# Optimization experiments

Measured on AMD Instinct MI355X. Metric: run time of the kernel, lower is better.

## Reference

```python
import jax, jax.numpy as jnp
import numpy as np

E = 384      # n_embed
H = 6        # n_head
HS = E // H  # head_size = 64
B = 64
T = 256      # == block_size
FF = 4 * E


def _layernorm(x, g, b, eps=1e-5):
    m = x.mean(-1, keepdims=True)
    v = ((x - m) ** 2).mean(-1, keepdims=True)
    return (x - m) / jnp.sqrt(v + eps) * g + b


def _mha(q_in, k_in, v_in, wq, bq, wk, bk, wv, bv, pw, pb):
    # Faithful to source: scale uses q_in's last dim (n_embed=384), NOT head_size,
    # and the causal tril mask is applied even in cross-attention.
    scale = q_in.shape[-1] ** -0.5
    q = jnp.einsum('bte,hes->bhts', q_in, wq) + bq[None, :, None, :]  # [B,H,T1,HS]
    k = jnp.einsum('bue,hes->bhus', k_in, wk) + bk[None, :, None, :]  # [B,H,T2,HS]
    v = jnp.einsum('bue,hes->bhus', v_in, wv) + bv[None, :, None, :]
    wei = jnp.einsum('bhts,bhus->bhtu', q, k) * scale                 # [B,H,T1,T2]
    T1, T2 = q_in.shape[1], k_in.shape[1]
    mask = jnp.tril(jnp.ones((T1, T2), dtype=bool))
    wei = jnp.where(mask[None, None], wei, -jnp.inf)
    wei = jax.nn.softmax(wei, axis=-1)
    out = jnp.einsum('bhtu,bhus->bths', wei, v)                       # [B,T1,H,HS]
    out = out.reshape(out.shape[0], out.shape[1], -1)                 # concat heads
    return out @ pw + pb


def setup_inputs() -> dict:
    key = jax.random.key(0)
    ks = jax.random.split(key, 32)
    s = 0.02
    d = {
        'encode_output': jax.random.normal(ks[0], (B, T, E), jnp.float32),
        'x': jax.random.normal(ks[1], (B, T, E), jnp.float32),
    }
    i = 2
    for p in ('sa1', 'sa2'):
        d[p + '_wq'] = jax.random.normal(ks[i], (H, E, HS), jnp.float32) * s; i += 1
        d[p + '_bq'] = jnp.zeros((H, HS), jnp.float32)
        d[p + '_wk'] = jax.random.normal(ks[i], (H, E, HS), jnp.float32) * s; i += 1
        d[p + '_bk'] = jnp.zeros((H, HS), jnp.float32)
        d[p + '_wv'] = jax.random.normal(ks[i], (H, E, HS), jnp.float32) * s; i += 1
        d[p + '_bv'] = jnp.zeros((H, HS), jnp.float32)
        d[p + '_pw'] = jax.random.normal(ks[i], (E, E), jnp.float32) * s; i += 1
        d[p + '_pb'] = jnp.zeros((E,), jnp.float32)
    d['ff_w1'] = jax.random.normal(ks[i], (E, FF), jnp.float32) * s; i += 1
    d['ff_b1'] = jnp.zeros((FF,), jnp.float32)
    d['ff_w2'] = jax.random.normal(ks[i], (FF, E), jnp.float32) * s; i += 1
    d['ff_b2'] = jnp.zeros((E,), jnp.float32)
    for n in ('ln1', 'ln2', 'ln3'):
        d[n + '_g'] = jnp.ones((E,), jnp.float32)
        d[n + '_b'] = jnp.zeros((E,), jnp.float32)
    return d


def reference(encode_output, x,
              sa1_wq, sa1_bq, sa1_wk, sa1_bk, sa1_wv, sa1_bv, sa1_pw, sa1_pb,
              sa2_wq, sa2_bq, sa2_wk, sa2_bk, sa2_wv, sa2_bv, sa2_pw, sa2_pb,
              ff_w1, ff_b1, ff_w2, ff_b2,
              ln1_g, ln1_b, ln2_g, ln2_b, ln3_g, ln3_b):
    # masked self-attention + add&norm
    a1 = _mha(x, x, x, sa1_wq, sa1_bq, sa1_wk, sa1_bk, sa1_wv, sa1_bv, sa1_pw, sa1_pb)
    o1 = _layernorm(x + a1, ln1_g, ln1_b)
    # cross-attention (q=o1, k=v=encode_output) + add&norm
    a2 = _mha(o1, encode_output, encode_output,
              sa2_wq, sa2_bq, sa2_wk, sa2_bk, sa2_wv, sa2_bv, sa2_pw, sa2_pb)
    o2 = _layernorm(o1 + a2, ln2_g, ln2_b)
    # FFN + add&norm
    f = jax.nn.relu(o2 @ ff_w1 + ff_b1) @ ff_w2 + ff_b2
    return _layernorm(o2 + f, ln3_g, ln3_b)
```

## Files before the change

kernel.cpp:

```cpp
#include <hip/hip_runtime.h>

typedef __attribute__((ext_vector_type(8))) short bf16x8;
typedef __attribute__((ext_vector_type(4))) float f32x4;

__device__ __forceinline__ float b2f(ushort b) {
    union { unsigned int u; float f; } x;
    x.u = ((unsigned int)b) << 16;
    return x.f;
}
__device__ __forceinline__ ushort f2b(float f) {
    union { float f; unsigned int u; } x;
    x.f = f;
    unsigned int r = x.u + 0x7fffu + ((x.u >> 16) & 1u);
    return (ushort)(r >> 16);
}
__device__ __forceinline__ int4 pack8(float4 a, float4 b) {
    union { int4 v; ushort u[8]; } r;
    r.u[0] = f2b(a.x); r.u[1] = f2b(a.y); r.u[2] = f2b(a.z); r.u[3] = f2b(a.w);
    r.u[4] = f2b(b.x); r.u[5] = f2b(b.y); r.u[6] = f2b(b.z); r.u[7] = f2b(b.w);
    return r.v;
}
__device__ __forceinline__ int4 add_resb(int4 cs, int4 rs) {
    const ushort* c = (const ushort*)&cs; const ushort* r = (const ushort*)&rs;
    union { int4 v; ushort u[8]; } o;
#pragma unroll
    for (int j = 0; j < 8; j++) o.u[j] = f2b(b2f(c[j]) + b2f(r[j]));
    return o.v;
}
__device__ __forceinline__ int4 add_resf(int4 cs, float4 r0, float4 r1) {
    const ushort* c = (const ushort*)&cs;
    const float* rf0 = (const float*)&r0; const float* rf1 = (const float*)&r1;
    union { int4 v; ushort u[8]; } o;
#pragma unroll
    for (int j = 0; j < 4; j++) o.u[j] = f2b(b2f(c[j]) + rf0[j]);
#pragma unroll
    for (int j = 0; j < 4; j++) o.u[4 + j] = f2b(b2f(c[4 + j]) + rf1[j]);
    return o.v;
}

__global__ __launch_bounds__(256) void gemm_bt(
    const ushort* __restrict__ A, const ushort* __restrict__ Bt,
    ushort* __restrict__ C, const float* __restrict__ bias,
    const ushort* __restrict__ resb, const float* __restrict__ resf,
    int N, int K, int relu)
{
    __shared__ __align__(16) ushort As[128 * 32];
    __shared__ __align__(16) ushort Bs[128 * 32];
    __shared__ __align__(16) ushort Cs[64 * 132];
    const int tid  = threadIdx.x;
    const int wave = tid >> 6, lane = tid & 63;
    const int wm = wave >> 1, wn = wave & 1;
    const int qd = lane >> 4, lc = lane & 15;
    const int id = blockIdx.x, xcd = id & 7, sub = id >> 3;
    const int row0 = (xcd * 16 + (sub & 15)) * 128;
    const int col0 = (sub >> 4) * 128;

    const int srow = tid >> 1;
    const int scol = (tid & 1) * 16;
    const ushort* Ag = A  + (size_t)(row0 + srow) * K + scol;
    const ushort* Bg = Bt + (size_t)(col0 + srow) * K + scol;
    ushort* Asd = &As[srow * 32 + scol];
    ushort* Bsd = &Bs[srow * 32 + scol];

    f32x4 acc[4][4];
#pragma unroll
    for (int i = 0; i < 4; i++)
#pragma unroll
        for (int j = 0; j < 4; j++) acc[i][j] = 0.0f;

    int4 a0 = *(const int4*)(Ag);
    int4 a1 = *(const int4*)(Ag + 8);
    int4 b0 = *(const int4*)(Bg);
    int4 b1 = *(const int4*)(Bg + 8);

    for (int k0 = 0; k0 < K; k0 += 32) {
        __syncthreads();
        *(int4*)Asd = a0; *(int4*)(Asd + 8) = a1;
        *(int4*)Bsd = b0; *(int4*)(Bsd + 8) = b1;
        if (k0 + 32 < K) {
            a0 = *(const int4*)(Ag + k0 + 32);
            a1 = *(const int4*)(Ag + k0 + 40);
            b0 = *(const int4*)(Bg + k0 + 32);
            b1 = *(const int4*)(Bg + k0 + 40);
        }
        __syncthreads();

        bf16x8 af[4], bfr[4];
#pragma unroll
        for (int mi = 0; mi < 4; mi++)
            af[mi] = *(const bf16x8*)&As[(wm * 64 + mi * 16 + lc) * 32 + qd * 8];
#pragma unroll
        for (int ni = 0; ni < 4; ni++)
            bfr[ni] = *(const bf16x8*)&Bs[(wn * 64 + ni * 16 + lc) * 32 + qd * 8];
#pragma unroll
        for (int mi = 0; mi < 4; mi++)
#pragma unroll
            for (int ni = 0; ni < 4; ni++)
                acc[mi][ni] = __builtin_amdgcn_mfma_f32_16x16x32_bf16(
                    af[mi], bfr[ni], acc[mi][ni], 0, 0, 0);
    }

#pragma unroll
    for (int half = 0; half < 2; half++) {
        __syncthreads();
        if (wm == half) {
#pragma unroll
            for (int mi = 0; mi < 4; mi++)
#pragma unroll
                for (int r = 0; r < 4; r++) {
                    int lr = mi * 16 + qd * 4 + r;
#pragma unroll
                    for (int ni = 0; ni < 4; ni++) {
                        float v = acc[mi][ni][r];
                        if (bias) v += bias[col0 + wn * 64 + ni * 16 + lc];
                        if (relu) v = fmaxf(v, 0.0f);
                        Cs[lr * 132 + wn * 64 + ni * 16 + lc] = f2b(v);
                    }
                }
        }
        __syncthreads();
        int lr = tid >> 2, cc = (tid & 3) * 32;
        size_t base = (size_t)(row0 + half * 64 + lr) * N + col0 + cc;
#pragma unroll
        for (int i = 0; i < 4; i++) {
            int4 d = *(const int4*)&Cs[lr * 132 + cc + i * 8];
            if (resb) d = add_resb(d, *(const int4*)&resb[base + i * 8]);
            else if (resf) d = add_resf(d, *(const float4*)&resf[base + i * 8],
                                           *(const float4*)&resf[base + i * 8 + 4]);
            *(int4*)&C[base + i * 8] = d;
        }
    }
}

__global__ __launch_bounds__(256) void gemm_n64(
    const ushort* __restrict__ A, const ushort* __restrict__ Bt,
    ushort* __restrict__ C, const float* __restrict__ bias,
    const ushort* __restrict__ resb, const float* __restrict__ resf,
    int N, int K, int relu)
{
    __shared__ __align__(16) ushort As[128 * 32];
    __shared__ __align__(16) ushort Bs[64 * 32];
    __shared__ __align__(16) ushort Cs[128 * 68];
    const int tid  = threadIdx.x;
    const int wave = tid >> 6, lane = tid & 63;
    const int qd = lane >> 4, lc = lane & 15;
    const int id = blockIdx.x, xcd = id & 7, sub = id >> 3;
    const int row0 = (xcd * 16 + (sub & 15)) * 128;
    const int col0 = (sub >> 4) * 64;

    const int srow = tid >> 1;
    const int scol = (tid & 1) * 16;
    const ushort* Ag = A + (size_t)(row0 + srow) * K + scol;
    ushort* Asd = &As[srow * 32 + scol];
    const int brow = tid >> 2;
    const int bcol = (tid & 3) * 8;
    const ushort* Bg = Bt + (size_t)(col0 + brow) * K + bcol;
    ushort* Bsd = &Bs[brow * 32 + bcol];

    f32x4 acc[2][4];
#pragma unroll
    for (int i = 0; i < 2; i++)
#pragma unroll
        for (int j = 0; j < 4; j++) acc[i][j] = 0.0f;

    int4 a0 = *(const int4*)(Ag);
    int4 a1 = *(const int4*)(Ag + 8);
    int4 b0 = *(const int4*)(Bg);

    for (int k0 = 0; k0 < K; k0 += 32) {
        __syncthreads();
        *(int4*)Asd = a0; *(int4*)(Asd + 8) = a1;
        *(int4*)Bsd = b0;
        if (k0 + 32 < K) {
            a0 = *(const int4*)(Ag + k0 + 32);
            a1 = *(const int4*)(Ag + k0 + 40);
            b0 = *(const int4*)(Bg + k0 + 32);
        }
        __syncthreads();

        bf16x8 af[2], bfr[4];
#pragma unroll
        for (int mi = 0; mi < 2; mi++)
            af[mi] = *(const bf16x8*)&As[(wave * 32 + mi * 16 + lc) * 32 + qd * 8];
#pragma unroll
        for (int ni = 0; ni < 4; ni++)
            bfr[ni] = *(const bf16x8*)&Bs[(ni * 16 + lc) * 32 + qd * 8];
#pragma unroll
        for (int mi = 0; mi < 2; mi++)
#pragma unroll
            for (int ni = 0; ni < 4; ni++)
                acc[mi][ni] = __builtin_amdgcn_mfma_f32_16x16x32_bf16(
                    af[mi], bfr[ni], acc[mi][ni], 0, 0, 0);
    }

    __syncthreads();
#pragma unroll
    for (int mi = 0; mi < 2; mi++)
#pragma unroll
        for (int r = 0; r < 4; r++) {
            int lr = wave * 32 + mi * 16 + qd * 4 + r;
#pragma unroll
            for (int ni = 0; ni < 4; ni++) {
                float v = acc[mi][ni][r];
                if (bias) v += bias[col0 + ni * 16 + lc];
                if (relu) v = fmaxf(v, 0.0f);
                Cs[lr * 68 + ni * 16 + lc] = f2b(v);
            }
        }
    __syncthreads();
    {
        int lr = tid >> 1, cc = (tid & 1) * 32;
        size_t base = (size_t)(row0 + lr) * N + col0 + cc;
#pragma unroll
        for (int i = 0; i < 4; i++) {
            int4 d = *(const int4*)&Cs[lr * 68 + cc + i * 8];
            if (resb) d = add_resb(d, *(const int4*)&resb[base + i * 8]);
            else if (resf) d = add_resf(d, *(const float4*)&resf[base + i * 8],
                                           *(const float4*)&resf[base + i * 8 + 4]);
            *(int4*)&C[base + i * 8] = d;
        }
    }
}

__global__ __launch_bounds__(256) void gemm_dual(
    const ushort* __restrict__ A1, const ushort* __restrict__ B1t,
    ushort* __restrict__ C1, const float* __restrict__ bias1, int N1,
    const ushort* __restrict__ A2, const ushort* __restrict__ B2t,
    ushort* __restrict__ C2, const float* __restrict__ bias2, int N2,
    int split, int K)
{
    __shared__ __align__(16) ushort As[128 * 32];
    __shared__ __align__(16) ushort Bs[64 * 32];
    __shared__ __align__(16) ushort Cs[128 * 68];
    const int tid  = threadIdx.x;
    const int wave = tid >> 6, lane = tid & 63;
    const int qd = lane >> 4, lc = lane & 15;
    const int id = blockIdx.x, xcd = id & 7, sub = id >> 3;
    const int row0 = (xcd * 16 + (sub & 15)) * 128;
    int ct = sub >> 4;
    const bool first = ct < split;
    const ushort* A  = first ? A1 : A2;
    const ushort* Bt = first ? B1t : B2t;
    ushort* C        = first ? C1 : C2;
    const float* bias = first ? bias1 : bias2;
    const int N      = first ? N1 : N2;
    const int col0   = (first ? ct : ct - split) * 64;

    const int srow = tid >> 1;
    const int scol = (tid & 1) * 16;
    const ushort* Ag = A + (size_t)(row0 + srow) * K + scol;
    ushort* Asd = &As[srow * 32 + scol];
    const int brow = tid >> 2;
    const int bcol = (tid & 3) * 8;
    const ushort* Bg = Bt + (size_t)(col0 + brow) * K + bcol;
    ushort* Bsd = &Bs[brow * 32 + bcol];

    f32x4 acc[2][4];
#pragma unroll
    for (int i = 0; i < 2; i++)
#pragma unroll
        for (int j = 0; j < 4; j++) acc[i][j] = 0.0f;

    int4 a0 = *(const int4*)(Ag);
    int4 a1 = *(const int4*)(Ag + 8);
    int4 b0 = *(const int4*)(Bg);

    for (int k0 = 0; k0 < K; k0 += 32) {
        __syncthreads();
        *(int4*)Asd = a0; *(int4*)(Asd + 8) = a1;
        *(int4*)Bsd = b0;
        if (k0 + 32 < K) {
            a0 = *(const int4*)(Ag + k0 + 32);
            a1 = *(const int4*)(Ag + k0 + 40);
            b0 = *(const int4*)(Bg + k0 + 32);
        }
        __syncthreads();

        bf16x8 af[2], bfr[4];
#pragma unroll
        for (int mi = 0; mi < 2; mi++)
            af[mi] = *(const bf16x8*)&As[(wave * 32 + mi * 16 + lc) * 32 + qd * 8];
#pragma unroll
        for (int ni = 0; ni < 4; ni++)
            bfr[ni] = *(const bf16x8*)&Bs[(ni * 16 + lc) * 32 + qd * 8];
#pragma unroll
        for (int mi = 0; mi < 2; mi++)
#pragma unroll
            for (int ni = 0; ni < 4; ni++)
                acc[mi][ni] = __builtin_amdgcn_mfma_f32_16x16x32_bf16(
                    af[mi], bfr[ni], acc[mi][ni], 0, 0, 0);
    }

    __syncthreads();
#pragma unroll
    for (int mi = 0; mi < 2; mi++)
#pragma unroll
        for (int r = 0; r < 4; r++) {
            int lr = wave * 32 + mi * 16 + qd * 4 + r;
#pragma unroll
            for (int ni = 0; ni < 4; ni++)
                Cs[lr * 68 + ni * 16 + lc] = f2b(acc[mi][ni][r] + bias[col0 + ni * 16 + lc]);
        }
    __syncthreads();
    {
        int lr = tid >> 1, cc = (tid & 1) * 32;
        size_t base = (size_t)(row0 + lr) * N + col0 + cc;
#pragma unroll
        for (int i = 0; i < 4; i++)
            *(int4*)&C[base + i * 8] = *(const int4*)&Cs[lr * 68 + cc + i * 8];
    }
}

__global__ __launch_bounds__(256) void attn(
    const ushort* __restrict__ q, int qstr,
    const ushort* __restrict__ k, int kstr,
    const ushort* __restrict__ v, int vstr,
    ushort* __restrict__ out)
{
    __shared__ __align__(16) ushort Qs[64 * 72];
    __shared__ __align__(16) ushort Kc[64 * 72];
    __shared__ __align__(16) ushort Vc[64 * 72];
    __shared__ __align__(16) ushort Ps[64 * 264];

    const int tid = threadIdx.x;
    const int wave = tid >> 6, lane = tid & 63;
    const int qd = lane >> 4, lc = lane & 15;
    const int b = blockIdx.z, h = blockIdx.y, t0 = blockIdx.x * 64;
    const int hc = h * 64;
    const float scale = 0.051031036307982884f;

    {
        int r = tid >> 2, c = (tid & 3) * 16;
        int4 q0 = *(const int4*)&q[(size_t)(b * 256 + t0 + r) * qstr + hc + c];
        int4 q1 = *(const int4*)&q[(size_t)(b * 256 + t0 + r) * qstr + hc + c + 8];
        *(int4*)&Qs[r * 72 + c] = q0;
        *(int4*)&Qs[r * 72 + c + 8] = q1;
    }

    f32x4 accS[16];
#pragma unroll
    for (int j = 0; j < 16; j++) accS[j] = 0.0f;

    for (int uc = 0; uc < 4; uc++) {
        int r = tid >> 2, c = (tid & 3) * 16;
        int4 k0v = *(const int4*)&k[(size_t)(b * 256 + uc * 64 + r) * kstr + hc + c];
        int4 k1v = *(const int4*)&k[(size_t)(b * 256 + uc * 64 + r) * kstr + hc + c + 8];
        __syncthreads();
        *(int4*)&Kc[r * 72 + c] = k0v;
        *(int4*)&Kc[r * 72 + c + 8] = k1v;
        __syncthreads();
#pragma unroll
        for (int s0 = 0; s0 < 64; s0 += 32) {
            bf16x8 a = *(const bf16x8*)&Qs[(wave * 16 + lc) * 72 + s0 + qd * 8];
#pragma unroll
            for (int ni = 0; ni < 4; ni++) {
                bf16x8 bb = *(const bf16x8*)&Kc[(ni * 16 + lc) * 72 + s0 + qd * 8];
                accS[uc * 4 + ni] =
                    __builtin_amdgcn_mfma_f32_16x16x32_bf16(a, bb, accS[uc * 4 + ni], 0, 0, 0);
            }
        }
    }

#pragma unroll
    for (int rr = 0; rr < 4; rr++) {
        int t = t0 + wave * 16 + qd * 4 + rr;
        float pv[16];
        float mx = -3.0e38f;
#pragma unroll
        for (int j = 0; j < 16; j++) {
            int u = (j >> 2) * 64 + (j & 3) * 16 + lc;
            float s = accS[j][rr] * scale;
            s = (u <= t) ? s : -3.0e38f;
            pv[j] = s;
            mx = fmaxf(mx, s);
        }
#pragma unroll
        for (int m = 1; m < 16; m <<= 1) mx = fmaxf(mx, __shfl_xor(mx, m, 16));
        float sum = 0.0f;
#pragma unroll
        for (int j = 0; j < 16; j++) { float p = __expf(pv[j] - mx); pv[j] = p; sum += p; }
#pragma unroll
        for (int m = 1; m < 16; m <<= 1) sum += __shfl_xor(sum, m, 16);
        float inv = 1.0f / sum;
#pragma unroll
        for (int j = 0; j < 16; j++) {
            int u = (j >> 2) * 64 + (j & 3) * 16 + lc;
            Ps[(wave * 16 + qd * 4 + rr) * 264 + u] = f2b(pv[j] * inv);
        }
    }

    f32x4 accO[4];
#pragma unroll
    for (int j = 0; j < 4; j++) accO[j] = 0.0f;
    for (int uc = 0; uc < 4; uc++) {
        int r = tid >> 2, s0 = (tid & 3) * 16;
        int4 v0 = *(const int4*)&v[(size_t)(b * 256 + uc * 64 + r) * vstr + hc + s0];
        int4 v1 = *(const int4*)&v[(size_t)(b * 256 + uc * 64 + r) * vstr + hc + s0 + 8];
        __syncthreads();
        {
            const ushort* t0p = (const ushort*)&v0;
            const ushort* t1p = (const ushort*)&v1;
#pragma unroll
            for (int j = 0; j < 8; j++) Vc[(s0 + j) * 72 + r] = t0p[j];
#pragma unroll
            for (int j = 0; j < 8; j++) Vc[(s0 + 8 + j) * 72 + r] = t1p[j];
        }
        __syncthreads();
#pragma unroll
        for (int u0 = 0; u0 < 64; u0 += 32) {
            bf16x8 a = *(const bf16x8*)&Ps[(wave * 16 + lc) * 264 + uc * 64 + u0 + qd * 8];
#pragma unroll
            for (int ni = 0; ni < 4; ni++) {
                bf16x8 bb = *(const bf16x8*)&Vc[(ni * 16 + lc) * 72 + u0 + qd * 8];
                accO[ni] = __builtin_amdgcn_mfma_f32_16x16x32_bf16(a, bb, accO[ni], 0, 0, 0);
            }
        }
    }

#pragma unroll
    for (int ni = 0; ni < 4; ni++)
#pragma unroll
        for (int rr = 0; rr < 4; rr++) {
            int t = t0 + wave * 16 + qd * 4 + rr;
            out[(size_t)(b * 256 + t) * 384 + hc + ni * 16 + lc] = f2b(accO[ni][rr]);
        }
}

__global__ __launch_bounds__(256) void lnorm(
    const ushort* __restrict__ in, const float* __restrict__ g,
    const float* __restrict__ be, ushort* __restrict__ outb,
    float* __restrict__ outf)
{
    const int wave = threadIdx.x >> 6, lane = threadIdx.x & 63;
    const int row = blockIdx.x * 4 + wave;
    const ushort* r = in + (size_t)row * 384;
    float x[6], s1 = 0.0f, s2 = 0.0f;
#pragma unroll
    for (int j = 0; j < 6; j++) {
        x[j] = b2f(r[j * 64 + lane]);
        s1 += x[j]; s2 += x[j] * x[j];
    }
#pragma unroll
    for (int m = 1; m < 64; m <<= 1) {
        s1 += __shfl_xor(s1, m, 64);
        s2 += __shfl_xor(s2, m, 64);
    }
    float mean = s1 * (1.0f / 384.0f);
    float var  = s2 * (1.0f / 384.0f) - mean * mean;
    float rstd = rsqrtf(var + 1e-5f);
#pragma unroll
    for (int j = 0; j < 6; j++) {
        float y = (x[j] - mean) * rstd * g[j * 64 + lane] + be[j * 64 + lane];
        if (outb) outb[(size_t)row * 384 + j * 64 + lane] = f2b(y);
        if (outf) outf[(size_t)row * 384 + j * 64 + lane] = y;
    }
}

__device__ __forceinline__ void dev_cvt(const float* in, ushort* out, int blk) {
    size_t i = ((size_t)blk * 256 + threadIdx.x) * 8;
    float4 a = *(const float4*)(in + i);
    float4 b = *(const float4*)(in + i + 4);
    *(int4*)(out + i) = pack8(a, b);
}
__device__ __forceinline__ void dev_transp(const float* in, ushort* out,
                                           int R, int C, int bx, int by,
                                           float (*t)[33]) {
    const int tx = threadIdx.x & 31, ty = threadIdx.x >> 5;
    const int c0 = bx * 32, r0 = by * 32;
#pragma unroll
    for (int i = 0; i < 32; i += 8)
        t[ty + i][tx] = in[(size_t)(r0 + ty + i) * C + c0 + tx];
    __syncthreads();
#pragma unroll
    for (int i = 0; i < 32; i += 8)
        out[(size_t)(c0 + ty + i) * R + r0 + tx] = f2b(t[tx][ty + i]);
}
__device__ __forceinline__ void dev_packqkv(const float* wq, const float* wk,
                                            const float* wv, ushort* Wt,
                                            int blk, float (*t)[33]) {
    const int tx = threadIdx.x & 31, ty = threadIdx.x >> 5;
    const int bx = blk % 12, by = (blk / 12) % 2, bz = blk / 24;
    const int e0 = bx * 32, s0 = by * 32;
    const int seg = bz / 6, h = bz - seg * 6;
    const float* w = (seg == 0) ? wq : (seg == 1) ? wk : wv;
    const float* wh = w + (size_t)h * 384 * 64;
#pragma unroll
    for (int i = 0; i < 32; i += 8)
        t[ty + i][tx] = wh[(size_t)(e0 + ty + i) * 64 + s0 + tx];
    __syncthreads();
    const int nbase = seg * 384 + h * 64 + s0;
#pragma unroll
    for (int i = 0; i < 32; i += 8)
        Wt[(size_t)(nbase + ty + i) * 384 + e0 + tx] = f2b(t[tx][ty + i]);
}

__global__ __launch_bounds__(256) void prep_all(
    const float* __restrict__ x, ushort* __restrict__ xb,
    const float* __restrict__ enc, ushort* __restrict__ encb,
    const float* __restrict__ s1wq, const float* __restrict__ s1wk,
    const float* __restrict__ s1wv, ushort* __restrict__ W1,
    const float* __restrict__ s2wq, const float* __restrict__ s2wk,
    const float* __restrict__ s2wv, ushort* __restrict__ W2,
    const float* __restrict__ s1pw, ushort* __restrict__ pw1t,
    const float* __restrict__ s2pw, ushort* __restrict__ pw2t,
    const float* __restrict__ fw1, ushort* __restrict__ w1t,
    const float* __restrict__ fw2, ushort* __restrict__ w2t,
    const float* __restrict__ s1bq, const float* __restrict__ s1bk,
    const float* __restrict__ s1bv, const float* __restrict__ s2bq,
    const float* __restrict__ s2bk, const float* __restrict__ s2bv,
    float* __restrict__ bias1, float* __restrict__ bias2)
{
    __shared__ float t[32][33];
    int blk = blockIdx.x;
    if (blk < 3072) { dev_cvt(x, xb, blk); return; }
    blk -= 3072;
    if (blk < 3072) { dev_cvt(enc, encb, blk); return; }
    blk -= 3072;
    if (blk < 432) { dev_packqkv(s1wq, s1wk, s1wv, W1, blk, t); return; }
    blk -= 432;
    if (blk < 432) { dev_packqkv(s2wq, s2wk, s2wv, W2, blk, t); return; }
    blk -= 432;
    if (blk < 144) { dev_transp(s1pw, pw1t, 384, 384, blk % 12, blk / 12, t); return; }
    blk -= 144;
    if (blk < 144) { dev_transp(s2pw, pw2t, 384, 384, blk % 12, blk / 12, t); return; }
    blk -= 144;
    if (blk < 576) { dev_transp(fw1, w1t, 384, 1536, blk % 48, blk / 48, t); return; }
    blk -= 576;
    if (blk < 576) { dev_transp(fw2, w2t, 1536, 384, blk % 12, blk / 12, t); return; }
    blk -= 576;
    int i = blk * 256 + threadIdx.x;
    if (i >= 2304) return;
    int grp = i / 1152, r = i - grp * 1152;
    int seg = r / 384, nn = r - seg * 384;
    const float* src = grp == 0 ? (seg == 0 ? s1bq : seg == 1 ? s1bk : s1bv)
                                : (seg == 0 ? s2bq : seg == 1 ? s2bk : s2bv);
    (grp == 0 ? bias1 : bias2)[r] = src[nn];
}

extern "C" void kernel_launch(void* const* d_in, const int* in_sizes, int n_in,
                              void* d_out, int out_size, void* d_ws, size_t ws_size,
                              hipStream_t stream)
{
    const float* enc = (const float*)d_in[0];
    const float* x   = (const float*)d_in[1];
    const float* s1wq = (const float*)d_in[2];  const float* s1bq = (const float*)d_in[3];
    const float* s1wk = (const float*)d_in[4];  const float* s1bk = (const float*)d_in[5];
    const float* s1wv = (const float*)d_in[6];  const float* s1bv = (const float*)d_in[7];
    const float* s1pw = (const float*)d_in[8];  const float* s1pb = (const float*)d_in[9];
    const float* s2wq = (const float*)d_in[10]; const float* s2bq = (const float*)d_in[11];
    const float* s2wk = (const float*)d_in[12]; const float* s2bk = (const float*)d_in[13];
    const float* s2wv = (const float*)d_in[14]; const float* s2bv = (const float*)d_in[15];
    const float* s2pw = (const float*)d_in[16]; const float* s2pb = (const float*)d_in[17];
    const float* fw1 = (const float*)d_in[18];  const float* fb1 = (const float*)d_in[19];
    const float* fw2 = (const float*)d_in[20];  const float* fb2 = (const float*)d_in[21];
    const float* g1 = (const float*)d_in[22];   const float* be1 = (const float*)d_in[23];
    const float* g2 = (const float*)d_in[24];   const float* be2 = (const float*)d_in[25];
    const float* g3 = (const float*)d_in[26];   const float* be3 = (const float*)d_in[27];

    if (ws_size < 80216064u) return;

    ushort* wsp = (ushort*)d_ws;
    ushort* qkv1 = wsp;
    ushort* q2   = wsp;
    ushort* kv2  = wsp + 6291456;
    ushort* h1   = wsp;
    ushort* att  = wsp + 18874368;
    ushort* xb   = wsp + 18874368;
    ushort* tmp  = wsp + 25165824;
    ushort* o1b  = wsp + 31457280;
    ushort* W1   = wsp + 37748736;
    ushort* W2   = W1 + 442368;
    ushort* pw1t = W2 + 442368;
    ushort* pw2t = pw1t + 147456;
    ushort* w1t  = pw2t + 147456;
    ushort* w2t  = w1t + 589824;

    ushort* encb = (ushort*)d_out;
    ushort* o2b  = (ushort*)d_out;
    float* bias1 = (float*)((ushort*)d_out + 6291456);
    float* bias2 = bias1 + 1152;

    prep_all<<<dim3(8457), dim3(256), 0, stream>>>(
        x, xb, enc, encb,
        s1wq, s1wk, s1wv, W1, s2wq, s2wk, s2wv, W2,
        s1pw, pw1t, s2pw, pw2t, fw1, w1t, fw2, w2t,
        s1bq, s1bk, s1bv, s2bq, s2bk, s2bv, bias1, bias2);

    gemm_bt<<<dim3(9 * 128), dim3(256), 0, stream>>>(xb, W1, qkv1, bias1, nullptr, nullptr, 1152, 384, 0);
    attn<<<dim3(4, 6, 64), dim3(256), 0, stream>>>(qkv1, 1152, qkv1 + 384, 1152, qkv1 + 768, 1152, att);
    gemm_n64<<<dim3(6 * 128), dim3(256), 0, stream>>>(att, pw1t, tmp, s1pb, nullptr, x, 384, 384, 0);
    lnorm<<<dim3(4096), dim3(256), 0, stream>>>(tmp, g1, be1, o1b, nullptr);

    gemm_dual<<<dim3(18 * 128), dim3(256), 0, stream>>>(
        o1b, W2, q2, bias2, 384,
        encb, W2 + 147456, kv2, bias2 + 384, 768, 6, 384);
    attn<<<dim3(4, 6, 64), dim3(256), 0, stream>>>(q2, 384, kv2, 768, kv2 + 384, 768, att);
    gemm_n64<<<dim3(6 * 128), dim3(256), 0, stream>>>(att, pw2t, tmp, s2pb, o1b, nullptr, 384, 384, 0);
    lnorm<<<dim3(4096), dim3(256), 0, stream>>>(tmp, g2, be2, o2b, nullptr);

    gemm_bt<<<dim3(12 * 128), dim3(256), 0, stream>>>(o2b, w1t, h1, fb1, nullptr, nullptr, 1536, 384, 1);
    gemm_n64<<<dim3(6 * 128), dim3(256), 0, stream>>>(h1, w2t, tmp, fb2, o2b, nullptr, 384, 1536, 0);
    lnorm<<<dim3(4096), dim3(256), 0, stream>>>(tmp, g3, be3, nullptr, (float*)d_out);
}
```

Baseline: 455.7 us.

## Use direct global-to-LDS loads with double-buffered K tiles in GEMMs

The three GEMM kernels stop staging A/B tiles through registers and instead issue global_load_lds so data goes straight into shared memory. Each kernel gets two LDS buffers and prefetches the next K tile while the current one feeds the MFMAs, using explicit vmcnt waits and raw barriers. The epilogue's output staging buffer is aliased onto the same LDS region. This removes the register round trip and the VGPR pressure of the prefetch, but leans on hand-counted vmcnt and barrier ordering for correctness.

```diff
diff --git a/kernel.cpp b/kernel.cpp
--- a/kernel.cpp
+++ b/kernel.cpp
@@ -36,6 +36,12 @@
 #pragma unroll
     for (int j = 0; j < 4; j++) o.u[4 + j] = f2b(b2f(c[4 + j]) + rf1[j]);
     return o.v;
+}
+
+__device__ __forceinline__ void gll16(const ushort* g, ushort* l) {
+    __builtin_amdgcn_global_load_lds(
+        (__attribute__((address_space(1))) void*)(g),
+        (__attribute__((address_space(3))) void*)(l), 16, 0, 0);
 }
 
 __global__ __launch_bounds__(256) void gemm_bt(
@@ -44,9 +50,7 @@
     const ushort* __restrict__ resb, const float* __restrict__ resf,
     int N, int K, int relu)
 {
-    __shared__ __align__(16) ushort As[128 * 32];
-    __shared__ __align__(16) ushort Bs[128 * 32];
-    __shared__ __align__(16) ushort Cs[64 * 132];
+    __shared__ __align__(16) ushort sm[16384];
     const int tid  = threadIdx.x;
     const int wave = tid >> 6, lane = tid & 63;
     const int wm = wave >> 1, wn = wave & 1;
@@ -55,12 +59,13 @@
     const int row0 = (xcd * 16 + (sub & 15)) * 128;
     const int col0 = (sub >> 4) * 128;
 
-    const int srow = tid >> 1;
-    const int scol = (tid & 1) * 16;
-    const ushort* Ag = A  + (size_t)(row0 + srow) * K + scol;
-    const ushort* Bg = Bt + (size_t)(col0 + srow) * K + scol;
-    ushort* Asd = &As[srow * 32 + scol];
-    ushort* Bsd = &Bs[srow * 32 + scol];
+    const int crow = lane >> 2, ccol = (lane & 3) * 8;
+    const ushort* Ag0 = A  + (size_t)(row0 + wave * 32 + crow) * K + ccol;
+    const ushort* Ag1 = Ag0 + (size_t)16 * K;
+    const ushort* Bg0 = Bt + (size_t)(col0 + wave * 32 + crow) * K + ccol;
+    const ushort* Bg1 = Bg0 + (size_t)16 * K;
+    ushort* dA = &sm[wave * 1024];
+    ushort* dB = &sm[4096 + wave * 1024];
 
     f32x4 acc[4][4];
 #pragma unroll
@@ -68,38 +73,43 @@
 #pragma unroll
         for (int j = 0; j < 4; j++) acc[i][j] = 0.0f;
 
-    int4 a0 = *(const int4*)(Ag);
-    int4 a1 = *(const int4*)(Ag + 8);
-    int4 b0 = *(const int4*)(Bg);
-    int4 b1 = *(const int4*)(Bg + 8);
-
-    for (int k0 = 0; k0 < K; k0 += 32) {
-        __syncthreads();
-        *(int4*)Asd = a0; *(int4*)(Asd + 8) = a1;
-        *(int4*)Bsd = b0; *(int4*)(Bsd + 8) = b1;
-        if (k0 + 32 < K) {
-            a0 = *(const int4*)(Ag + k0 + 32);
-            a1 = *(const int4*)(Ag + k0 + 40);
-            b0 = *(const int4*)(Bg + k0 + 32);
-            b1 = *(const int4*)(Bg + k0 + 40);
-        }
-        __syncthreads();
-
+    gll16(Ag0, dA); gll16(Ag1, dA + 512);
+    gll16(Bg0, dB); gll16(Bg1, dB + 512);
+
+    const int NT = K >> 5;
+    int cur = 0;
+    for (int t = 0; t < NT; ++t) {
+        __builtin_amdgcn_s_barrier();
+        if (t + 1 < NT) {
+            const int ko = (t + 1) << 5;
+            const int bo = (cur ^ 1) * 8192;
+            gll16(Ag0 + ko, dA + bo); gll16(Ag1 + ko, dA + bo + 512);
+            gll16(Bg0 + ko, dB + bo); gll16(Bg1 + ko, dB + bo + 512);
+            asm volatile("s_waitcnt vmcnt(4)" ::: "memory");
+        } else {
+            asm volatile("s_waitcnt vmcnt(0)" ::: "memory");
+        }
+        __builtin_amdgcn_s_barrier();
+
+        const ushort* Ac = &sm[cur * 8192];
+        const ushort* Bc = &sm[cur * 8192 + 4096];
         bf16x8 af[4], bfr[4];
 #pragma unroll
         for (int mi = 0; mi < 4; mi++)
-            af[mi] = *(const bf16x8*)&As[(wm * 64 + mi * 16 + lc) * 32 + qd * 8];
+            af[mi] = *(const bf16x8*)&Ac[(wm * 64 + mi * 16 + lc) * 32 + qd * 8];
 #pragma unroll
         for (int ni = 0; ni < 4; ni++)
-            bfr[ni] = *(const bf16x8*)&Bs[(wn * 64 + ni * 16 + lc) * 32 + qd * 8];
+            bfr[ni] = *(const bf16x8*)&Bc[(wn * 64 + ni * 16 + lc) * 32 + qd * 8];
 #pragma unroll
         for (int mi = 0; mi < 4; mi++)
 #pragma unroll
             for (int ni = 0; ni < 4; ni++)
                 acc[mi][ni] = __builtin_amdgcn_mfma_f32_16x16x32_bf16(
                     af[mi], bfr[ni], acc[mi][ni], 0, 0, 0);
-    }
-
+        cur ^= 1;
+    }
+
+    ushort* Cs = sm;
 #pragma unroll
     for (int half = 0; half < 2; half++) {
         __syncthreads();
@@ -138,9 +148,7 @@
     const ushort* __restrict__ resb, const float* __restrict__ resf,
     int N, int K, int relu)
 {
-    __shared__ __align__(16) ushort As[128 * 32];
-    __shared__ __align__(16) ushort Bs[64 * 32];
-    __shared__ __align__(16) ushort Cs[128 * 68];
+    __shared__ __align__(16) ushort sm[12288];
     const int tid  = threadIdx.x;
     const int wave = tid >> 6, lane = tid & 63;
     const int qd = lane >> 4, lc = lane & 15;
@@ -148,14 +156,12 @@
     const int row0 = (xcd * 16 + (sub & 15)) * 128;
     const int col0 = (sub >> 4) * 64;
 
-    const int srow = tid >> 1;
-    const int scol = (tid & 1) * 16;
-    const ushort* Ag = A + (size_t)(row0 + srow) * K + scol;
-    ushort* Asd = &As[srow * 32 + scol];
-    const int brow = tid >> 2;
-    const int bcol = (tid & 3) * 8;
-    const ushort* Bg = Bt + (size_t)(col0 + brow) * K + bcol;
-    ushort* Bsd = &Bs[brow * 32 + bcol];
+    const int crow = lane >> 2, ccol = (lane & 3) * 8;
+    const ushort* Ag0 = A  + (size_t)(row0 + wave * 32 + crow) * K + ccol;
+    const ushort* Ag1 = Ag0 + (size_t)16 * K;
+    const ushort* Bg0 = Bt + (size_t)(col0 + wave * 16 + crow) * K + ccol;
+    ushort* dA = &sm[wave * 1024];
+    ushort* dB = &sm[4096 + wave * 512];
 
     f32x4 acc[2][4];
 #pragma unroll
@@ -163,36 +169,43 @@
 #pragma unroll
         for (int j = 0; j < 4; j++) acc[i][j] = 0.0f;
 
-    int4 a0 = *(const int4*)(Ag);
-    int4 a1 = *(const int4*)(Ag + 8);
-    int4 b0 = *(const int4*)(Bg);
-
-    for (int k0 = 0; k0 < K; k0 += 32) {
-        __syncthreads();
-        *(int4*)Asd = a0; *(int4*)(Asd + 8) = a1;
-        *(int4*)Bsd = b0;
-        if (k0 + 32 < K) {
-            a0 = *(const int4*)(Ag + k0 + 32);
-            a1 = *(const int4*)(Ag + k0 + 40);
-            b0 = *(const int4*)(Bg + k0 + 32);
-        }
-        __syncthreads();
-
+    gll16(Ag0, dA); gll16(Ag1, dA + 512);
+    gll16(Bg0, dB);
+
+    const int NT = K >> 5;
+    int cur = 0;
+    for (int t = 0; t < NT; ++t) {
+        __builtin_amdgcn_s_barrier();
+        if (t + 1 < NT) {
+            const int ko = (t + 1) << 5;
+            const int bo = (cur ^ 1) * 6144;
+            gll16(Ag0 + ko, dA + bo); gll16(Ag1 + ko, dA + bo + 512);
+            gll16(Bg0 + ko, dB + bo);
+            asm volatile("s_waitcnt vmcnt(3)" ::: "memory");
+        } else {
+            asm volatile("s_waitcnt vmcnt(0)" ::: "memory");
+        }
+        __builtin_amdgcn_s_barrier();
+
+        const ushort* Ac = &sm[cur * 6144];
+        const ushort* Bc = &sm[cur * 6144 + 4096];
         bf16x8 af[2], bfr[4];
 #pragma unroll
         for (int mi = 0; mi < 2; mi++)
-            af[mi] = *(const bf16x8*)&As[(wave * 32 + mi * 16 + lc) * 32 + qd * 8];
+            af[mi] = *(const bf16x8*)&Ac[(wave * 32 + mi * 16 + lc) * 32 + qd * 8];
 #pragma unroll
         for (int ni = 0; ni < 4; ni++)
-            bfr[ni] = *(const bf16x8*)&Bs[(ni * 16 + lc) * 32 + qd * 8];
+            bfr[ni] = *(const bf16x8*)&Bc[(ni * 16 + lc) * 32 + qd * 8];
 #pragma unroll
         for (int mi = 0; mi < 2; mi++)
 #pragma unroll
             for (int ni = 0; ni < 4; ni++)
                 acc[mi][ni] = __builtin_amdgcn_mfma_f32_16x16x32_bf16(
                     af[mi], bfr[ni], acc[mi][ni], 0, 0, 0);
-    }
-
+        cur ^= 1;
+    }
+
+    ushort* Cs = sm;
     __syncthreads();
 #pragma unroll
     for (int mi = 0; mi < 2; mi++)
@@ -229,9 +242,7 @@
     ushort* __restrict__ C2, const float* __restrict__ bias2, int N2,
     int split, int K)
 {
-    __shared__ __align__(16) ushort As[128 * 32];
-    __shared__ __align__(16) ushort Bs[64 * 32];
-    __shared__ __align__(16) ushort Cs[128 * 68];
+    __shared__ __align__(16) ushort sm[12288];
     const int tid  = threadIdx.x;
     const int wave = tid >> 6, lane = tid & 63;
     const int qd = lane >> 4, lc = lane & 15;
@@ -246,14 +257,12 @@
     const int N      = first ? N1 : N2;
     const int col0   = (first ? ct : ct - split) * 64;
 
-    const int srow = tid >> 1;
-    const int scol = (tid & 1) * 16;
-    const ushort* Ag = A + (size_t)(row0 + srow) * K + scol;
-    ushort* Asd = &As[srow * 32 + scol];
-    const int brow = tid >> 2;
-    const int bcol = (tid & 3) * 8;
-    const ushort* Bg = Bt + (size_t)(col0 + brow) * K + bcol;
-    ushort* Bsd = &Bs[brow * 32 + bcol];
+    const int crow = lane >> 2, ccol = (lane & 3) * 8;
+    const ushort* Ag0 = A  + (size_t)(row0 + wave * 32 + crow) * K + ccol;
+    const ushort* Ag1 = Ag0 + (size_t)16 * K;
+    const ushort* Bg0 = Bt + (size_t)(col0 + wave * 16 + crow) * K + ccol;
+    ushort* dA = &sm[wave * 1024];
+    ushort* dB = &sm[4096 + wave * 512];
 
     f32x4 acc[2][4];
 #pragma unroll
@@ -261,36 +270,43 @@
 #pragma unroll
         for (int j = 0; j < 4; j++) acc[i][j] = 0.0f;
 
-    int4 a0 = *(const int4*)(Ag);
-    int4 a1 = *(const int4*)(Ag + 8);
-    int4 b0 = *(const int4*)(Bg);
-
-    for (int k0 = 0; k0 < K; k0 += 32) {
-        __syncthreads();
-        *(int4*)Asd = a0; *(int4*)(Asd + 8) = a1;
-        *(int4*)Bsd = b0;
-        if (k0 + 32 < K) {
-            a0 = *(const int4*)(Ag + k0 + 32);
-            a1 = *(const int4*)(Ag + k0 + 40);
-            b0 = *(const int4*)(Bg + k0 + 32);
-        }
-        __syncthreads();
-
+    gll16(Ag0, dA); gll16(Ag1, dA + 512);
+    gll16(Bg0, dB);
+
+    const int NT = K >> 5;
+    int cur = 0;
+    for (int t = 0; t < NT; ++t) {
+        __builtin_amdgcn_s_barrier();
+        if (t + 1 < NT) {
+            const int ko = (t + 1) << 5;
+            const int bo = (cur ^ 1) * 6144;
+            gll16(Ag0 + ko, dA + bo); gll16(Ag1 + ko, dA + bo + 512);
+            gll16(Bg0 + ko, dB + bo);
+            asm volatile("s_waitcnt vmcnt(3)" ::: "memory");
+        } else {
+            asm volatile("s_waitcnt vmcnt(0)" ::: "memory");
+        }
+        __builtin_amdgcn_s_barrier();
+
+        const ushort* Ac = &sm[cur * 6144];
+        const ushort* Bc = &sm[cur * 6144 + 4096];
         bf16x8 af[2], bfr[4];
 #pragma unroll
         for (int mi = 0; mi < 2; mi++)
-            af[mi] = *(const bf16x8*)&As[(wave * 32 + mi * 16 + lc) * 32 + qd * 8];
+            af[mi] = *(const bf16x8*)&Ac[(wave * 32 + mi * 16 + lc) * 32 + qd * 8];
 #pragma unroll
         for (int ni = 0; ni < 4; ni++)
-            bfr[ni] = *(const bf16x8*)&Bs[(ni * 16 + lc) * 32 + qd * 8];
+            bfr[ni] = *(const bf16x8*)&Bc[(ni * 16 + lc) * 32 + qd * 8];
 #pragma unroll
         for (int mi = 0; mi < 2; mi++)
 #pragma unroll
             for (int ni = 0; ni < 4; ni++)
                 acc[mi][ni] = __builtin_amdgcn_mfma_f32_16x16x32_bf16(
                     af[mi], bfr[ni], acc[mi][ni], 0, 0, 0);
-    }
-
+        cur ^= 1;
+    }
+
+    ushort* Cs = sm;
     __syncthreads();
 #pragma unroll
     for (int mi = 0; mi < 2; mi++)
```

Result: no change. 452.0 us (-0.8%).

## Rewrite GEMMs to stage full-K weight slab in LDS via direct global loads

Applied to the files above, without the earlier changes.

Replaces the per-32-K double-buffered A/B LDS tiling with a scheme that loads a 64-column weight slab covering 384 K into LDS through global_load_lds. A fragments are read straight from global memory into registers. Each wave now writes its own epilogue tile, so the block-wide barrier before the store goes away, and MFMA sections get raised scheduling priority. This cuts per-K-step barriers and LDS traffic for A, at the cost of uncoalesced, possibly latency-exposed A loads from global memory and larger LDS use per block.

```diff
diff --git a/kernel.cpp b/kernel.cpp
--- a/kernel.cpp
+++ b/kernel.cpp
@@ -38,206 +38,114 @@
     return o.v;
 }
 
-__global__ __launch_bounds__(256) void gemm_bt(
+__device__ __forceinline__ void gll16(const ushort* g, ushort* l) {
+    __builtin_amdgcn_global_load_lds(
+        (__attribute__((address_space(1))) void*)(g),
+        (__attribute__((address_space(3))) void*)(l), 16, 0, 0);
+}
+
+template<int MI>
+__global__ __launch_bounds__(256) void gemm_bs(
     const ushort* __restrict__ A, const ushort* __restrict__ Bt,
     ushort* __restrict__ C, const float* __restrict__ bias,
     const ushort* __restrict__ resb, const float* __restrict__ resf,
     int N, int K, int relu)
 {
-    __shared__ __align__(16) ushort As[128 * 32];
-    __shared__ __align__(16) ushort Bs[128 * 32];
-    __shared__ __align__(16) ushort Cs[64 * 132];
-    const int tid  = threadIdx.x;
-    const int wave = tid >> 6, lane = tid & 63;
-    const int wm = wave >> 1, wn = wave & 1;
-    const int qd = lane >> 4, lc = lane & 15;
-    const int id = blockIdx.x, xcd = id & 7, sub = id >> 3;
-    const int row0 = (xcd * 16 + (sub & 15)) * 128;
-    const int col0 = (sub >> 4) * 128;
-
-    const int srow = tid >> 1;
-    const int scol = (tid & 1) * 16;
-    const ushort* Ag = A  + (size_t)(row0 + srow) * K + scol;
-    const ushort* Bg = Bt + (size_t)(col0 + srow) * K + scol;
-    ushort* Asd = &As[srow * 32 + scol];
-    ushort* Bsd = &Bs[srow * 32 + scol];
-
-    f32x4 acc[4][4];
-#pragma unroll
-    for (int i = 0; i < 4; i++)
-#pragma unroll
-        for (int j = 0; j < 4; j++) acc[i][j] = 0.0f;
-
-    int4 a0 = *(const int4*)(Ag);
-    int4 a1 = *(const int4*)(Ag + 8);
-    int4 b0 = *(const int4*)(Bg);
-    int4 b1 = *(const int4*)(Bg + 8);
-
-    for (int k0 = 0; k0 < K; k0 += 32) {
-        __syncthreads();
-        *(int4*)Asd = a0; *(int4*)(Asd + 8) = a1;
-        *(int4*)Bsd = b0; *(int4*)(Bsd + 8) = b1;
-        if (k0 + 32 < K) {
-            a0 = *(const int4*)(Ag + k0 + 32);
-            a1 = *(const int4*)(Ag + k0 + 40);
-            b0 = *(const int4*)(Bg + k0 + 32);
-            b1 = *(const int4*)(Bg + k0 + 40);
-        }
-        __syncthreads();
-
-        bf16x8 af[4], bfr[4];
-#pragma unroll
-        for (int mi = 0; mi < 4; mi++)
-            af[mi] = *(const bf16x8*)&As[(wm * 64 + mi * 16 + lc) * 32 + qd * 8];
-#pragma unroll
-        for (int ni = 0; ni < 4; ni++)
-            bfr[ni] = *(const bf16x8*)&Bs[(wn * 64 + ni * 16 + lc) * 32 + qd * 8];
-#pragma unroll
-        for (int mi = 0; mi < 4; mi++)
-#pragma unroll
-            for (int ni = 0; ni < 4; ni++)
-                acc[mi][ni] = __builtin_amdgcn_mfma_f32_16x16x32_bf16(
-                    af[mi], bfr[ni], acc[mi][ni], 0, 0, 0);
-    }
-
-#pragma unroll
-    for (int half = 0; half < 2; half++) {
-        __syncthreads();
-        if (wm == half) {
-#pragma unroll
-            for (int mi = 0; mi < 4; mi++)
-#pragma unroll
-                for (int r = 0; r < 4; r++) {
-                    int lr = mi * 16 + qd * 4 + r;
-#pragma unroll
-                    for (int ni = 0; ni < 4; ni++) {
-                        float v = acc[mi][ni][r];
-                        if (bias) v += bias[col0 + wn * 64 + ni * 16 + lc];
-                        if (relu) v = fmaxf(v, 0.0f);
-                        Cs[lr * 132 + wn * 64 + ni * 16 + lc] = f2b(v);
-                    }
-                }
-        }
-        __syncthreads();
-        int lr = tid >> 2, cc = (tid & 3) * 32;
-        size_t base = (size_t)(row0 + half * 64 + lr) * N + col0 + cc;
-#pragma unroll
-        for (int i = 0; i < 4; i++) {
-            int4 d = *(const int4*)&Cs[lr * 132 + cc + i * 8];
-            if (resb) d = add_resb(d, *(const int4*)&resb[base + i * 8]);
-            else if (resf) d = add_resf(d, *(const float4*)&resf[base + i * 8],
-                                           *(const float4*)&resf[base + i * 8 + 4]);
-            *(int4*)&C[base + i * 8] = d;
-        }
-    }
-}
-
-__global__ __launch_bounds__(256) void gemm_n64(
-    const ushort* __restrict__ A, const ushort* __restrict__ Bt,
-    ushort* __restrict__ C, const float* __restrict__ bias,
-    const ushort* __restrict__ resb, const float* __restrict__ resf,
-    int N, int K, int relu)
-{
-    __shared__ __align__(16) ushort As[128 * 32];
-    __shared__ __align__(16) ushort Bs[64 * 32];
-    __shared__ __align__(16) ushort Cs[128 * 68];
+    __shared__ __align__(16) ushort sm[24576];
+    constexpr int CHUNK = MI * 64;
+    constexpr int PERX  = (16384 / CHUNK) / 8;
     const int tid  = threadIdx.x;
     const int wave = tid >> 6, lane = tid & 63;
     const int qd = lane >> 4, lc = lane & 15;
     const int id = blockIdx.x, xcd = id & 7, sub = id >> 3;
-    const int row0 = (xcd * 16 + (sub & 15)) * 128;
-    const int col0 = (sub >> 4) * 64;
-
-    const int srow = tid >> 1;
-    const int scol = (tid & 1) * 16;
-    const ushort* Ag = A + (size_t)(row0 + srow) * K + scol;
-    ushort* Asd = &As[srow * 32 + scol];
-    const int brow = tid >> 2;
-    const int bcol = (tid & 3) * 8;
-    const ushort* Bg = Bt + (size_t)(col0 + brow) * K + bcol;
-    ushort* Bsd = &Bs[brow * 32 + bcol];
-
-    f32x4 acc[2][4];
-#pragma unroll
-    for (int i = 0; i < 2; i++)
+    const int mc = sub % PERX, ct = sub / PERX;
+    const int row0 = (xcd * PERX + mc) * CHUNK;
+    const int col0 = ct * 64;
+
+    f32x4 acc[MI][4];
+#pragma unroll
+    for (int i = 0; i < MI; i++)
 #pragma unroll
         for (int j = 0; j < 4; j++) acc[i][j] = 0.0f;
 
-    int4 a0 = *(const int4*)(Ag);
-    int4 a1 = *(const int4*)(Ag + 8);
-    int4 b0 = *(const int4*)(Bg);
-
-    for (int k0 = 0; k0 < K; k0 += 32) {
+    const ushort* Aw = A + (size_t)(row0 + wave * MI * 16 + lc) * K + qd * 8;
+    const ushort* Bw = Bt + (size_t)(col0 + wave * 16 + (lane >> 2)) * K + (lane & 3) * 8;
+    ushort* Bsw = &sm[wave * 512];
+
+    const int NKC = K / 384;
+    for (int kc = 0; kc < NKC; ++kc) {
+        if (kc) __syncthreads();
+#pragma unroll
+        for (int j = 0; j < 12; j++)
+            gll16(Bw + kc * 384 + j * 32, Bsw + j * 2048);
         __syncthreads();
-        *(int4*)Asd = a0; *(int4*)(Asd + 8) = a1;
-        *(int4*)Bsd = b0;
-        if (k0 + 32 < K) {
-            a0 = *(const int4*)(Ag + k0 + 32);
-            a1 = *(const int4*)(Ag + k0 + 40);
-            b0 = *(const int4*)(Bg + k0 + 32);
-        }
-        __syncthreads();
-
-        bf16x8 af[2], bfr[4];
-#pragma unroll
-        for (int mi = 0; mi < 2; mi++)
-            af[mi] = *(const bf16x8*)&As[(wave * 32 + mi * 16 + lc) * 32 + qd * 8];
-#pragma unroll
-        for (int ni = 0; ni < 4; ni++)
-            bfr[ni] = *(const bf16x8*)&Bs[(ni * 16 + lc) * 32 + qd * 8];
-#pragma unroll
-        for (int mi = 0; mi < 2; mi++)
+
+        const ushort* Akc = Aw + kc * 384;
+#pragma unroll
+        for (int kk = 0; kk < 12; ++kk) {
+            bf16x8 af[MI];
+#pragma unroll
+            for (int mi = 0; mi < MI; mi++)
+                af[mi] = *(const bf16x8*)(Akc + (size_t)mi * 16 * K + kk * 32);
+            bf16x8 bfr[4];
 #pragma unroll
             for (int ni = 0; ni < 4; ni++)
-                acc[mi][ni] = __builtin_amdgcn_mfma_f32_16x16x32_bf16(
-                    af[mi], bfr[ni], acc[mi][ni], 0, 0, 0);
+                bfr[ni] = *(const bf16x8*)&sm[kk * 2048 + (ni * 16 + lc) * 32 + qd * 8];
+            __builtin_amdgcn_s_setprio(1);
+#pragma unroll
+            for (int mi = 0; mi < MI; mi++)
+#pragma unroll
+                for (int ni = 0; ni < 4; ni++)
+                    acc[mi][ni] = __builtin_amdgcn_mfma_f32_16x16x32_bf16(
+                        af[mi], bfr[ni], acc[mi][ni], 0, 0, 0);
+            __builtin_amdgcn_s_setprio(0);
+        }
     }
 
     __syncthreads();
-#pragma unroll
-    for (int mi = 0; mi < 2; mi++)
+    ushort* Csw = &sm[wave * MI * 16 * 68];
+#pragma unroll
+    for (int mi = 0; mi < MI; mi++)
 #pragma unroll
         for (int r = 0; r < 4; r++) {
-            int lr = wave * 32 + mi * 16 + qd * 4 + r;
+            int lr = mi * 16 + qd * 4 + r;
 #pragma unroll
             for (int ni = 0; ni < 4; ni++) {
                 float v = acc[mi][ni][r];
                 if (bias) v += bias[col0 + ni * 16 + lc];
                 if (relu) v = fmaxf(v, 0.0f);
-                Cs[lr * 68 + ni * 16 + lc] = f2b(v);
+                Csw[lr * 68 + ni * 16 + lc] = f2b(v);
             }
         }
-    __syncthreads();
-    {
-        int lr = tid >> 1, cc = (tid & 1) * 32;
-        size_t base = (size_t)(row0 + lr) * N + col0 + cc;
-#pragma unroll
-        for (int i = 0; i < 4; i++) {
-            int4 d = *(const int4*)&Cs[lr * 68 + cc + i * 8];
-            if (resb) d = add_resb(d, *(const int4*)&resb[base + i * 8]);
-            else if (resf) d = add_resf(d, *(const float4*)&resf[base + i * 8],
-                                           *(const float4*)&resf[base + i * 8 + 4]);
-            *(int4*)&C[base + i * 8] = d;
-        }
-    }
-}
-
-__global__ __launch_bounds__(256) void gemm_dual(
+    asm volatile("s_waitcnt lgkmcnt(0)" ::: "memory");
+    const int rowW = row0 + wave * MI * 16;
+#pragma unroll
+    for (int p = 0; p < MI * 2; p++) {
+        int lr = p * 8 + (lane >> 3), cc = (lane & 7) * 8;
+        size_t base = (size_t)(rowW + lr) * N + col0 + cc;
+        int4 d = *(const int4*)&Csw[lr * 68 + cc];
+        if (resb) d = add_resb(d, *(const int4*)&resb[base]);
+        else if (resf) d = add_resf(d, *(const float4*)&resf[base],
+                                       *(const float4*)&resf[base + 4]);
+        *(int4*)&C[base] = d;
+    }
+}
+
+__global__ __launch_bounds__(256) void gemm_bs_dual(
     const ushort* __restrict__ A1, const ushort* __restrict__ B1t,
     ushort* __restrict__ C1, const float* __restrict__ bias1, int N1,
     const ushort* __restrict__ A2, const ushort* __restrict__ B2t,
     ushort* __restrict__ C2, const float* __restrict__ bias2, int N2,
-    int split, int K)
+    int split)
 {
-    __shared__ __align__(16) ushort As[128 * 32];
-    __shared__ __align__(16) ushort Bs[64 * 32];
-    __shared__ __align__(16) ushort Cs[128 * 68];
+    __shared__ __align__(16) ushort sm[24576];
+    const int K = 384;
     const int tid  = threadIdx.x;
     const int wave = tid >> 6, lane = tid & 63;
     const int qd = lane >> 4, lc = lane & 15;
     const int id = blockIdx.x, xcd = id & 7, sub = id >> 3;
-    const int row0 = (xcd * 16 + (sub & 15)) * 128;
-    int ct = sub >> 4;
+    const int mc = sub & 15, ct = sub >> 4;
+    const int row0 = (xcd * 16 + mc) * 128;
     const bool first = ct < split;
     const ushort* A  = first ? A1 : A2;
     const ushort* Bt = first ? B1t : B2t;
@@ -246,68 +154,59 @@
     const int N      = first ? N1 : N2;
     const int col0   = (first ? ct : ct - split) * 64;
 
-    const int srow = tid >> 1;
-    const int scol = (tid & 1) * 16;
-    const ushort* Ag = A + (size_t)(row0 + srow) * K + scol;
-    ushort* Asd = &As[srow * 32 + scol];
-    const int brow = tid >> 2;
-    const int bcol = (tid & 3) * 8;
-    const ushort* Bg = Bt + (size_t)(col0 + brow) * K + bcol;
-    ushort* Bsd = &Bs[brow * 32 + bcol];
-
     f32x4 acc[2][4];
 #pragma unroll
     for (int i = 0; i < 2; i++)
 #pragma unroll
         for (int j = 0; j < 4; j++) acc[i][j] = 0.0f;
 
-    int4 a0 = *(const int4*)(Ag);
-    int4 a1 = *(const int4*)(Ag + 8);
-    int4 b0 = *(const int4*)(Bg);
-
-    for (int k0 = 0; k0 < K; k0 += 32) {
-        __syncthreads();
-        *(int4*)Asd = a0; *(int4*)(Asd + 8) = a1;
-        *(int4*)Bsd = b0;
-        if (k0 + 32 < K) {
-            a0 = *(const int4*)(Ag + k0 + 32);
-            a1 = *(const int4*)(Ag + k0 + 40);
-            b0 = *(const int4*)(Bg + k0 + 32);
-        }
-        __syncthreads();
-
-        bf16x8 af[2], bfr[4];
+    const ushort* Aw = A + (size_t)(row0 + wave * 32 + lc) * K + qd * 8;
+    const ushort* Bw = Bt + (size_t)(col0 + wave * 16 + (lane >> 2)) * K + (lane & 3) * 8;
+    ushort* Bsw = &sm[wave * 512];
+
+#pragma unroll
+    for (int j = 0; j < 12; j++)
+        gll16(Bw + j * 32, Bsw + j * 2048);
+    __syncthreads();
+
+#pragma unroll
+    for (int kk = 0; kk < 12; ++kk) {
+        bf16x8 af[2];
 #pragma unroll
         for (int mi = 0; mi < 2; mi++)
-            af[mi] = *(const bf16x8*)&As[(wave * 32 + mi * 16 + lc) * 32 + qd * 8];
+            af[mi] = *(const bf16x8*)(Aw + (size_t)mi * 16 * K + kk * 32);
+        bf16x8 bfr[4];
 #pragma unroll
         for (int ni = 0; ni < 4; ni++)
-            bfr[ni] = *(const bf16x8*)&Bs[(ni * 16 + lc) * 32 + qd * 8];
+            bfr[ni] = *(const bf16x8*)&sm[kk * 2048 + (ni * 16 + lc) * 32 + qd * 8];
+        __builtin_amdgcn_s_setprio(1);
 #pragma unroll
         for (int mi = 0; mi < 2; mi++)
 #pragma unroll
             for (int ni = 0; ni < 4; ni++)
                 acc[mi][ni] = __builtin_amdgcn_mfma_f32_16x16x32_bf16(
                     af[mi], bfr[ni], acc[mi][ni], 0, 0, 0);
+        __builtin_amdgcn_s_setprio(0);
     }
 
     __syncthreads();
+    ushort* Csw = &sm[wave * 32 * 68];
 #pragma unroll
     for (int mi = 0; mi < 2; mi++)
 #pragma unroll
         for (int r = 0; r < 4; r++) {
-            int lr = wave * 32 + mi * 16 + qd * 4 + r;
+            int lr = mi * 16 + qd * 4 + r;
 #pragma unroll
             for (int ni = 0; ni < 4; ni++)
-                Cs[lr * 68 + ni * 16 + lc] = f2b(acc[mi][ni][r] + bias[col0 + ni * 16 + lc]);
-        }
-    __syncthreads();
-    {
-        int lr = tid >> 1, cc = (tid & 1) * 32;
-        size_t base = (size_t)(row0 + lr) * N + col0 + cc;
-#pragma unroll
-        for (int i = 0; i < 4; i++)
-            *(int4*)&C[base + i * 8] = *(const int4*)&Cs[lr * 68 + cc + i * 8];
+                Csw[lr * 68 + ni * 16 + lc] = f2b(acc[mi][ni][r] + bias[col0 + ni * 16 + lc]);
+        }
+    asm volatile("s_waitcnt lgkmcnt(0)" ::: "memory");
+    const int rowW = row0 + wave * 32;
+#pragma unroll
+    for (int p = 0; p < 4; p++) {
+        int lr = p * 8 + (lane >> 3), cc = (lane & 7) * 8;
+        size_t base = (size_t)(rowW + lr) * N + col0 + cc;
+        *(int4*)&C[base] = *(const int4*)&Csw[lr * 68 + cc];
     }
 }
 
@@ -586,19 +485,26 @@
         s1pw, pw1t, s2pw, pw2t, fw1, w1t, fw2, w2t,
         s1bq, s1bk, s1bv, s2bq, s2bk, s2bv, bias1, bias2);
 
-    gemm_bt<<<dim3(9 * 128), dim3(256), 0, stream>>>(xb, W1, qkv1, bias1, nullptr, nullptr, 1152, 384, 0);
-    attn<<<dim3(4, 6, 64), dim3(256), 0, stream>>>(qkv1, 1152, qkv1 + 384, 1152, qkv1 + 768, 1152, att);
-    gemm_n64<<<dim3(6 * 128), dim3(256), 0, stream>>>(att, pw1t, tmp, s1pb, nullptr, x, 384, 384, 0);
+    gemm_bs<4><<<dim3(1152), dim3(256), 0, stream>>>(
+        xb, W1, qkv1, bias1, nullptr, nullptr, 1152, 384, 0);
+    attn<<<dim3(4, 6, 64), dim3(256), 0, stream>>>(
+        qkv1, 1152, qkv1 + 384, 1152, qkv1 + 768, 1152, att);
+    gemm_bs<2><<<dim3(768), dim3(256), 0, stream>>>(
+        att, pw1t, tmp, s1pb, nullptr, x, 384, 384, 0);
     lnorm<<<dim3(4096), dim3(256), 0, stream>>>(tmp, g1, be1, o1b, nullptr);
 
-    gemm_dual<<<dim3(18 * 128), dim3(256), 0, stream>>>(
+    gemm_bs_dual<<<dim3(2304), dim3(256), 0, stream>>>(
         o1b, W2, q2, bias2, 384,
-        encb, W2 + 147456, kv2, bias2 + 384, 768, 6, 384);
-    attn<<<dim3(4, 6, 64), dim3(256), 0, stream>>>(q2, 384, kv2, 768, kv2 + 384, 768, att);
-    gemm_n64<<<dim3(6 * 128), dim3(256), 0, stream>>>(att, pw2t, tmp, s2pb, o1b, nullptr, 384, 384, 0);
+        encb, W2 + 147456, kv2, bias2 + 384, 768, 6);
+    attn<<<dim3(4, 6, 64), dim3(256), 0, stream>>>(
+        q2, 384, kv2, 768, kv2 + 384, 768, att);
+    gemm_bs<2><<<dim3(768), dim3(256), 0, stream>>>(
+        att, pw2t, tmp, s2pb, o1b, nullptr, 384, 384, 0);
     lnorm<<<dim3(4096), dim3(256), 0, stream>>>(tmp, g2, be2, o2b, nullptr);
 
-    gemm_bt<<<dim3(12 * 128), dim3(256), 0, stream>>>(o2b, w1t, h1, fb1, nullptr, nullptr, 1536, 384, 1);
-    gemm_n64<<<dim3(6 * 128), dim3(256), 0, stream>>>(h1, w2t, tmp, fb2, o2b, nullptr, 384, 1536, 0);
+    gemm_bs<4><<<dim3(1536), dim3(256), 0, stream>>>(
+        o2b, w1t, h1, fb1, nullptr, nullptr, 1536, 384, 1);
+    gemm_bs<2><<<dim3(768), dim3(256), 0, stream>>>(
+        h1, w2t, tmp, fb2, o2b, nullptr, 384, 1536, 0);
     lnorm<<<dim3(4096), dim3(256), 0, stream>>>(tmp, g3, be3, nullptr, (float*)d_out);
 }
```

New measurement: 468.5 us. 1.03x slower.
